# Kernel optimization log

Measured on AMD Instinct MI355X. Metric: run time of the kernel, lower is better.

## Reference

```python
import jax, jax.numpy as jnp
import numpy as np

N = 50000
E = 800000
H = 128


def _lin_init(key, fan_in, fan_out):
    s = 1.0 / np.sqrt(fan_in)
    k1, k2 = jax.random.split(key)
    W = jax.random.uniform(k1, (fan_in, fan_out), minval=-s, maxval=s, dtype=jnp.float32)
    b = jax.random.uniform(k2, (fan_out,), minval=-s, maxval=s, dtype=jnp.float32)
    return W, b


def setup_inputs() -> dict:
    key = jax.random.key(0)
    ks = jax.random.split(key, 24)
    inp = {}
    inp['x'] = jax.random.normal(ks[0], (N, 1), dtype=jnp.float32)
    inp['edge_attr'] = jax.random.normal(ks[1], (E, 1), dtype=jnp.float32)
    inp['q_Y_sample'] = jax.random.normal(ks[2], (E, 1), dtype=jnp.float32)
    inp['adj'] = jax.random.randint(ks[3], (2, E), 0, N, dtype=jnp.int32)
    inp['t'] = jax.random.uniform(ks[4], (1,), dtype=jnp.float32) * 1000.0
    inp['num_steps'] = 1000
    inp['batch'] = jnp.zeros((N,), dtype=jnp.int32)
    # parameters
    inp['We'], inp['be'] = _lin_init(ks[5], 1, H // 2)      # edge_map
    inp['Wo'], inp['bo'] = _lin_init(ks[6], 1, H // 2)      # edge_map_opt
    inp['Wl1'], inp['bl1'] = _lin_init(ks[7], H, 1)         # conv1 edge lin (edge_dim->in_channels)
    inp['Wn1'], inp['bn1'] = _lin_init(ks[8], 1, H)         # conv1 nn
    inp['Wl2'], inp['bl2'] = _lin_init(ks[9], H, H)         # conv2 edge lin
    inp['Wn2'], inp['bn2'] = _lin_init(ks[10], H, H)        # conv2 nn
    inp['Wl3'], inp['bl3'] = _lin_init(ks[11], H, H)        # conv3 edge lin
    inp['Wn3'], inp['bn3'] = _lin_init(ks[12], H, H)        # conv3 nn
    inp['Wt1'], inp['bt1'] = _lin_init(ks[13], H, 2 * H)    # time_mlp[0]
    inp['Wt2'], inp['bt2'] = _lin_init(ks[14], 2 * H, H)    # time_mlp[2]
    inp['Wd1'], inp['bd1'] = _lin_init(ks[15], 257, 257)    # decode[0]
    inp['Wd2'], inp['bd2'] = _lin_init(ks[16], 257, 1)      # decode[2]
    return inp


def reference(x, edge_attr, q_Y_sample, adj, t, num_steps, batch,
              We, be, Wo, bo,
              Wl1, bl1, Wn1, bn1, Wl2, bl2, Wn2, bn2, Wl3, bl3, Wn3, bn3,
              Wt1, bt1, Wt2, bt2, Wd1, bd1, Wd2, bd2):
    n = x.shape[0]
    src, dst = adj[0], adj[1]
    # edge embedding: cat(edge_map(edge_attr), edge_map_opt(q_Y_sample)) -> [E, 128]
    ee = jnp.concatenate([edge_attr @ We + be, q_Y_sample @ Wo + bo], axis=-1)
    # sinusoidal time embedding (t/num_steps*num_steps*rescale == 4*t)
    half = H // 2
    freqs = jnp.exp(jnp.arange(half, dtype=jnp.float32) * (-np.log(10000.0) / (half - 1)))
    tv = (t * 4.0)[:, None] * freqs[None, :]
    temb = jnp.concatenate([jnp.sin(tv), jnp.cos(tv)], axis=-1)  # [1, 128]
    temb = jax.nn.relu(temb @ Wt1 + bt1) @ Wt2 + bt2              # [1, 128], broadcasts to [N, 128]

    def gine(h, Wl, bl, Wn, bn):
        # PyG GINEConv (eps=0): out = nn(x + sum_j relu(x_j + lin(edge_attr)))
        m = jax.nn.relu(h[src] + (ee @ Wl + bl))                  # [E, d_in]
        agg = jax.ops.segment_sum(m, dst, num_segments=n)         # [N, d_in]
        return (h + agg) @ Wn + bn

    h = gine(x, Wl1, bl1, Wn1, bn1) + temb
    h = gine(h, Wl2, bl2, Wn2, bn2) + temb
    h = gine(h, Wl3, bl3, Wn3, bn3) + temb
    # decode on edges: cat(h[src], h[dst], q_Y_sample) -> MLP -> [E, 1]
    z = jnp.concatenate([h[src], h[dst], q_Y_sample], axis=-1)    # [E, 257]
    return jax.nn.relu(z @ Wd1 + bd1) @ Wd2 + bd2
```

## Files before the change

kernel.cpp:

```cpp
#include <hip/hip_runtime.h>

typedef unsigned int uint;
typedef unsigned short ushort;

#define AB_U 132

typedef __attribute__((ext_vector_type(8))) short short8;
typedef __attribute__((ext_vector_type(4))) float f32x4;
union U4S8 { uint4 u; short8 s; };

__device__ __forceinline__ ushort f2bf(float f) {
    uint u = __float_as_uint(f);
    u += 0x7FFFu + ((u >> 16) & 1u);
    return (ushort)(u >> 16);
}
__device__ __forceinline__ float bf2f_lo(uint p) { return __uint_as_float(p << 16); }
__device__ __forceinline__ float bf2f_hi(uint p) { return __uint_as_float(p & 0xFFFF0000u); }
__device__ __forceinline__ uint packbf(float lo, float hi) {
    return (uint)f2bf(lo) | ((uint)f2bf(hi) << 16);
}

__global__ __launch_bounds__(256) void precompute_kernel(
    const float* __restrict__ t,
    const float* __restrict__ We, const float* __restrict__ be,
    const float* __restrict__ Wo, const float* __restrict__ bo,
    const float* __restrict__ Wl1, const float* __restrict__ bl1,
    const float* __restrict__ Wl2, const float* __restrict__ bl2,
    const float* __restrict__ Wl3, const float* __restrict__ bl3,
    const float* __restrict__ Wt1, const float* __restrict__ bt1,
    const float* __restrict__ Wt2, const float* __restrict__ bt2,
    float* __restrict__ wsmall)
{
    __shared__ float t0[128];
    __shared__ float y1[256];
    int tid = threadIdx.x;
    float tt = t[0] * 4.0f;
    if (tid < 64) {
        float f = expf(-logf(10000.0f) * (float)tid / 63.0f);
        float v = tt * f;
        t0[tid]      = sinf(v);
        t0[tid + 64] = cosf(v);
    }
    __syncthreads();
    {
        float acc = bt1[tid];
        for (int k = 0; k < 128; k++) acc = fmaf(t0[k], Wt1[k * 256 + tid], acc);
        y1[tid] = fmaxf(acc, 0.0f);
    }
    __syncthreads();
    if (tid < 128) {
        float a = bt2[tid];
        for (int k = 0; k < 256; k++) a = fmaf(y1[k], Wt2[k * 128 + tid], a);
        wsmall[tid] = a;
    }
    {
        int j = tid & 127;
        const float* Wl  = (tid < 128) ? Wl2 : Wl3;
        const float* blp = (tid < 128) ? bl2 : bl3;
        float p = 0.f, q = 0.f, r = blp[j];
        for (int k = 0; k < 64; k++) {
            float w1 = Wl[k * 128 + j], w2 = Wl[(64 + k) * 128 + j];
            p = fmaf(We[k], w1, p);
            q = fmaf(Wo[k], w2, q);
            r = fmaf(be[k], w1, r);
            r = fmaf(bo[k], w2, r);
        }
        int base = (tid < 128) ? 128 : 512;
        wsmall[base + j]       = p;
        wsmall[base + 128 + j] = q;
        wsmall[base + 256 + j] = r;
    }
    if (tid == 0) {
        float p1 = 0.f, q1 = 0.f, r1 = bl1[0];
        for (int k = 0; k < 64; k++) {
            p1 = fmaf(We[k], Wl1[k], p1);
            q1 = fmaf(Wo[k], Wl1[64 + k], q1);
            r1 = fmaf(be[k], Wl1[k], r1);
            r1 = fmaf(bo[k], Wl1[64 + k], r1);
        }
        wsmall[896] = p1; wsmall[897] = q1; wsmall[898] = r1;
    }
}

__global__ __launch_bounds__(64) void wt16_kernel(
    const float* __restrict__ Wd1, uint* __restrict__ Wt16u)
{
    int c = blockIdx.x;
    int u = threadIdx.x;
    int k = u * 2;
    float lo, hi;
    if (c < 256) {
        lo = Wd1[k * 257 + c];
        hi = Wd1[(k + 1) * 257 + c];
    } else {
        int cc = c - 256;
        lo = Wd1[(128 + k) * 257 + cc];
        hi = Wd1[(128 + k + 1) * 257 + cc];
    }
    Wt16u[c * 64 + u] = packbf(lo, hi);
}

__global__ __launch_bounds__(64) void wnt16_kernel(
    const float* __restrict__ W, uint* __restrict__ Wt)
{
    int c = blockIdx.x, u = threadIdx.x;
    Wt[c * 64 + u] = packbf(W[(2 * u) * 128 + c], W[(2 * u + 1) * 128 + c]);
}

__global__ __launch_bounds__(256) void hist_kernel(
    const int* __restrict__ dst, int* __restrict__ cnt, int E)
{
    int e = blockIdx.x * blockDim.x + threadIdx.x;
    if (e < E) atomicAdd(&cnt[dst[e]], 1);
}

__global__ __launch_bounds__(256) void scan1_kernel(
    const int* __restrict__ cnt, int* __restrict__ rowstart,
    int* __restrict__ partials, int N)
{
    __shared__ int wsum[4];
    int b = blockIdx.x;
    int tid = threadIdx.x, lane = tid & 63, w = tid >> 6;
    int i0 = b * 1024 + tid * 4;
    int v0 = (i0     < N) ? cnt[i0]     : 0;
    int v1 = (i0 + 1 < N) ? cnt[i0 + 1] : 0;
    int v2 = (i0 + 2 < N) ? cnt[i0 + 2] : 0;
    int v3 = (i0 + 3 < N) ? cnt[i0 + 3] : 0;
    int tsum = v0 + v1 + v2 + v3;
    int s = tsum;
#pragma unroll
    for (int off = 1; off < 64; off <<= 1) {
        int u = __shfl_up(s, off, 64);
        if (lane >= off) s += u;
    }
    if (lane == 63) wsum[w] = s;
    __syncthreads();
    int woff = 0;
    for (int k = 0; k < w; k++) woff += wsum[k];
    int ex = woff + s - tsum;
    if (i0     < N) rowstart[i0]     = ex;
    if (i0 + 1 < N) rowstart[i0 + 1] = ex + v0;
    if (i0 + 2 < N) rowstart[i0 + 2] = ex + v0 + v1;
    if (i0 + 3 < N) rowstart[i0 + 3] = ex + v0 + v1 + v2;
    if (tid == 255) partials[b] = woff + s;
}

__global__ __launch_bounds__(64) void scan2_kernel(
    int* __restrict__ partials, int* __restrict__ rowstart, int nblk, int N)
{
    int lane = threadIdx.x;
    int carry = 0;
    for (int base = 0; base < nblk; base += 64) {
        int i = base + lane;
        int v = (i < nblk) ? partials[i] : 0;
        int s = v;
#pragma unroll
        for (int off = 1; off < 64; off <<= 1) {
            int u = __shfl_up(s, off, 64);
            if (lane >= off) s += u;
        }
        if (i < nblk) partials[i] = carry + s - v;
        carry += __shfl(s, 63, 64);
    }
    if (lane == 0) rowstart[N] = carry;
}

__global__ __launch_bounds__(256) void scan3_kernel(
    int* __restrict__ rowstart, const int* __restrict__ partials, int N)
{
    int i = blockIdx.x * blockDim.x + threadIdx.x;
    if (i < N) rowstart[i] += partials[i >> 10];
}

__global__ __launch_bounds__(256) void scatter_kernel(
    const int* __restrict__ src, const int* __restrict__ dst,
    const float* __restrict__ ea, const float* __restrict__ qy,
    const int* __restrict__ rowstart, int* __restrict__ cursor,
    uint4* __restrict__ epack, int E)
{
    int e = blockIdx.x * blockDim.x + threadIdx.x;
    if (e >= E) return;
    int d = dst[e];
    int pos = atomicAdd(&cursor[d], 1);
    uint4 pk;
    pk.x = (uint)e;
    pk.y = (uint)src[e];
    pk.z = __float_as_uint(ea[e]);
    pk.w = __float_as_uint(qy[e]);
    epack[rowstart[d] + pos] = pk;
}

__global__ __launch_bounds__(256) void edge1_kernel(
    const float* __restrict__ x, const uint4* __restrict__ epack,
    const int* __restrict__ rowstart, const float* __restrict__ scal,
    float* __restrict__ agg1, int N)
{
    int v = blockIdx.x * blockDim.x + threadIdx.x;
    if (v >= N) return;
    float s0 = scal[0], s1 = scal[1], s2 = scal[2];
    int beg = rowstart[v], end = rowstart[v + 1];
    float m = 0.0f;
    int i = beg;
    for (; i + 2 <= end; i += 2) {
        uint4 pk0 = epack[i];
        uint4 pk1 = epack[i + 1];
        float x0 = x[(int)pk0.y];
        float x1 = x[(int)pk1.y];
        m += fmaxf(x0 + fmaf(__uint_as_float(pk0.z), s0, fmaf(__uint_as_float(pk0.w), s1, s2)), 0.0f);
        m += fmaxf(x1 + fmaf(__uint_as_float(pk1.z), s0, fmaf(__uint_as_float(pk1.w), s1, s2)), 0.0f);
    }
    if (i < end) {
        uint4 pk = epack[i];
        m += fmaxf(x[(int)pk.y] + fmaf(__uint_as_float(pk.z), s0, fmaf(__uint_as_float(pk.w), s1, s2)), 0.0f);
    }
    agg1[v] = m;
}

__global__ __launch_bounds__(256) void node1_kernel(
    const float* __restrict__ x, const float* __restrict__ agg1,
    const float* __restrict__ Wn1, const float* __restrict__ bn1,
    const float* __restrict__ temb, uint* __restrict__ h16u, int N)
{
    int i = blockIdx.x * blockDim.x + threadIdx.x;
    int n = i >> 6, j2 = (i & 63) * 2;
    if (n >= N) return;
    float v = x[n] + agg1[n];
    float h0 = fmaf(v, Wn1[j2],     bn1[j2]     + temb[j2]);
    float h1 = fmaf(v, Wn1[j2 + 1], bn1[j2 + 1] + temb[j2 + 1]);
    h16u[(size_t)n * 64 + (j2 >> 1)] = packbf(h0, h1);
}

__global__ __launch_bounds__(256) void aggL_kernel(
    const uint* __restrict__ h16u, const uint4* __restrict__ epack,
    const int* __restrict__ rowstart,
    const float* __restrict__ P, const float* __restrict__ Q,
    const float* __restrict__ R, uint* __restrict__ agg16u, int N)
{
    int v = blockIdx.x * 4 + (threadIdx.x >> 6);
    int lane = threadIdx.x & 63;
    if (v >= N) return;
    int c = lane * 2;
    float2 Pv = *(const float2*)(P + c);
    float2 Qv = *(const float2*)(Q + c);
    float2 Rv = *(const float2*)(R + c);
    int beg = rowstart[v], end = rowstart[v + 1];
    float accx = 0.0f, accy = 0.0f;
    int i = beg;
    for (; i + 8 <= end; i += 8) {
        uint4 pk[8];
        uint hp[8];
#pragma unroll
        for (int j = 0; j < 8; j++) pk[j] = epack[i + j];
#pragma unroll
        for (int j = 0; j < 8; j++) hp[j] = h16u[(size_t)pk[j].y * 64 + lane];
#pragma unroll
        for (int j = 0; j < 8; j++) {
            float a = __uint_as_float(pk[j].z), b = __uint_as_float(pk[j].w);
            accx += fmaxf(bf2f_lo(hp[j]) + fmaf(a, Pv.x, fmaf(b, Qv.x, Rv.x)), 0.0f);
            accy += fmaxf(bf2f_hi(hp[j]) + fmaf(a, Pv.y, fmaf(b, Qv.y, Rv.y)), 0.0f);
        }
    }
    for (; i + 2 <= end; i += 2) {
        uint4 pk0 = epack[i];
        uint4 pk1 = epack[i + 1];
        uint hp0 = h16u[(size_t)pk0.y * 64 + lane];
        uint hp1 = h16u[(size_t)pk1.y * 64 + lane];
        float a0 = __uint_as_float(pk0.z), b0 = __uint_as_float(pk0.w);
        float a1 = __uint_as_float(pk1.z), b1 = __uint_as_float(pk1.w);
        accx += fmaxf(bf2f_lo(hp0) + fmaf(a0, Pv.x, fmaf(b0, Qv.x, Rv.x)), 0.0f);
        accy += fmaxf(bf2f_hi(hp0) + fmaf(a0, Pv.y, fmaf(b0, Qv.y, Rv.y)), 0.0f);
        accx += fmaxf(bf2f_lo(hp1) + fmaf(a1, Pv.x, fmaf(b1, Qv.x, Rv.x)), 0.0f);
        accy += fmaxf(bf2f_hi(hp1) + fmaf(a1, Pv.y, fmaf(b1, Qv.y, Rv.y)), 0.0f);
    }
    if (i < end) {
        uint4 pk = epack[i];
        float a = __uint_as_float(pk.z), b = __uint_as_float(pk.w);
        uint hp = h16u[(size_t)pk.y * 64 + lane];
        accx += fmaxf(bf2f_lo(hp) + fmaf(a, Pv.x, fmaf(b, Qv.x, Rv.x)), 0.0f);
        accy += fmaxf(bf2f_hi(hp) + fmaf(a, Pv.y, fmaf(b, Qv.y, Rv.y)), 0.0f);
    }
    agg16u[(size_t)v * 64 + lane] = packbf(accx, accy);
}

__global__ __launch_bounds__(256) void nodeL_kernel(
    const uint* __restrict__ agg16u, const uint* __restrict__ Wn2t16u,
    const float* __restrict__ bn, const float* __restrict__ temb,
    uint* __restrict__ h16u, int N)
{
    __shared__ uint vs16[64][68];
    int nb = blockIdx.x * 64;
    int tid = threadIdx.x;
    for (int idx = tid; idx < 64 * 32; idx += 256) {
        int n = idx >> 5, u2 = (idx & 31) * 2;
        uint2 pk = make_uint2(0, 0);
        if (nb + n < N) {
            uint2 hp = *(const uint2*)(h16u + (size_t)(nb + n) * 64 + u2);
            uint2 gp = *(const uint2*)(agg16u + (size_t)(nb + n) * 64 + u2);
            pk.x = packbf(bf2f_lo(hp.x) + bf2f_lo(gp.x), bf2f_hi(hp.x) + bf2f_hi(gp.x));
            pk.y = packbf(bf2f_lo(hp.y) + bf2f_lo(gp.y), bf2f_hi(hp.y) + bf2f_hi(gp.y));
        }
        *(uint2*)(&vs16[n][u2]) = pk;
    }
    __syncthreads();
    int wv = tid >> 6, lane = tid & 63, cl = lane & 15, g = lane >> 4;
    int rbase = wv * 16;
    short8 afr[4];
#pragma unroll
    for (int kc = 0; kc < 4; kc++) {
        U4S8 t;
        t.u = *(const uint4*)(&vs16[rbase + cl][kc * 16 + g * 4]);
        afr[kc] = t.s;
    }
#pragma unroll
    for (int tt = 0; tt < 8; tt++) {
        int c = tt * 16 + cl;
        float bias = bn[c] + temb[c];
        f32x4 acc = {bias, bias, bias, bias};
#pragma unroll
        for (int kc = 0; kc < 4; kc++) {
            U4S8 t;
            t.u = *(const uint4*)(Wn2t16u + (size_t)c * 64 + kc * 16 + g * 4);
            acc = __builtin_amdgcn_mfma_f32_16x16x32_bf16(afr[kc], t.s, acc, 0, 0, 0);
        }
#pragma unroll
        for (int r = 0; r < 4; r++) {
            int n = nb + rbase + g * 4 + r;
            float val = acc[r];
            float nbr = __shfl_down(val, 1, 64);
            if (n < N && (cl & 1) == 0)
                h16u[(size_t)n * 64 + (c >> 1)] = packbf(val, nbr);
        }
    }
}

__global__ __launch_bounds__(256) void node3_decode_kernel(
    const uint* __restrict__ h16u, const uint* __restrict__ agg16u,
    const uint* __restrict__ Wn3t16u, const float* __restrict__ bn3,
    const float* __restrict__ temb, const uint* __restrict__ Wt16u,
    const float* __restrict__ Wd1, const float* __restrict__ bd1,
    uint* __restrict__ A16u, uint* __restrict__ B16u, int N)
{
    __shared__ uint vs16[16][68];
    __shared__ float hs3[16][132];
    __shared__ uint stA[16 * 132];
    __shared__ uint stB[16 * 132];
    int nb = blockIdx.x * 16;
    int tid = threadIdx.x;
    for (int idx = tid; idx < 16 * 32; idx += 256) {
        int n = idx >> 5, u2 = (idx & 31) * 2;
        uint2 pk = make_uint2(0, 0);
        if (nb + n < N) {
            uint2 hp = *(const uint2*)(h16u + (size_t)(nb + n) * 64 + u2);
            uint2 gp = *(const uint2*)(agg16u + (size_t)(nb + n) * 64 + u2);
            pk.x = packbf(bf2f_lo(hp.x) + bf2f_lo(gp.x), bf2f_hi(hp.x) + bf2f_hi(gp.x));
            pk.y = packbf(bf2f_lo(hp.y) + bf2f_lo(gp.y), bf2f_hi(hp.y) + bf2f_hi(gp.y));
        }
        *(uint2*)(&vs16[n][u2]) = pk;
    }
    __syncthreads();
    int wv = tid >> 6, lane = tid & 63, cl = lane & 15, g = lane >> 4;
    {
        short8 afr[4];
#pragma unroll
        for (int kc = 0; kc < 4; kc++) {
            U4S8 t;
            t.u = *(const uint4*)(&vs16[cl][kc * 16 + g * 4]);
            afr[kc] = t.s;
        }
#pragma unroll
        for (int tt = 0; tt < 2; tt++) {
            int c = wv * 32 + tt * 16 + cl;
            float bias = bn3[c] + temb[c];
            f32x4 acc = {bias, bias, bias, bias};
#pragma unroll
            for (int kc = 0; kc < 4; kc++) {
                U4S8 t;
                t.u = *(const uint4*)(Wn3t16u + (size_t)c * 64 + kc * 16 + g * 4);
                acc = __builtin_amdgcn_mfma_f32_16x16x32_bf16(afr[kc], t.s, acc, 0, 0, 0);
            }
#pragma unroll
            for (int r = 0; r < 4; r++) hs3[g * 4 + r][c] = acc[r];
        }
    }
    __syncthreads();
    {
        short8 afr[4];
#pragma unroll
        for (int kc = 0; kc < 4; kc++) {
            float4 lo = *(const float4*)(&hs3[cl][kc * 32 + g * 8]);
            float4 hi = *(const float4*)(&hs3[cl][kc * 32 + g * 8 + 4]);
            U4S8 t;
            t.u.x = packbf(lo.x, lo.y);
            t.u.y = packbf(lo.z, lo.w);
            t.u.z = packbf(hi.x, hi.y);
            t.u.w = packbf(hi.z, hi.w);
            afr[kc] = t.s;
        }
#pragma unroll
        for (int tt = 0; tt < 8; tt++) {
            int tile = wv * 8 + tt;
            int c = tile * 16 + cl;
            float bias = (tile < 16) ? bd1[c] : 0.0f;
            f32x4 acc = {bias, bias, bias, bias};
#pragma unroll
            for (int kc = 0; kc < 4; kc++) {
                U4S8 t;
                t.u = *(const uint4*)(Wt16u + (size_t)c * 64 + kc * 16 + g * 4);
                acc = __builtin_amdgcn_mfma_f32_16x16x32_bf16(afr[kc], t.s, acc, 0, 0, 0);
            }
            ushort* SP = (ushort*)((tile < 16) ? stA : stB);
            int oc = (tile < 16) ? c : (c - 256);
#pragma unroll
            for (int r = 0; r < 4; r++)
                SP[(g * 4 + r) * 264 + oc] = f2bf(acc[r]);
        }
    }
    if (tid < 64) {
        int n = tid >> 2, j = tid & 3;
        float sA = 0.f, sB = 0.f;
        for (int k = j * 32; k < j * 32 + 32; k++) {
            float hv = hs3[n][k];
            sA = fmaf(hv, Wd1[k * 257 + 256], sA);
            sB = fmaf(hv, Wd1[(128 + k) * 257 + 256], sB);
        }
        sA += __shfl_xor(sA, 1, 64);
        sA += __shfl_xor(sA, 2, 64);
        sB += __shfl_xor(sB, 1, 64);
        sB += __shfl_xor(sB, 2, 64);
        if (j == 0) {
            ((ushort*)stA)[n * 264 + 256] = f2bf(sA + bd1[256]);
            ((ushort*)stB)[n * 264 + 256] = f2bf(sB);
        }
    }
    __syncthreads();
    {
        int rows = N - nb; if (rows > 16) rows = 16;
        int tot2 = rows * 66;
        uint2* gA = (uint2*)(A16u + (size_t)nb * AB_U);
        uint2* gB = (uint2*)(B16u + (size_t)nb * AB_U);
        const uint2* sA = (const uint2*)stA;
        const uint2* sB = (const uint2*)stB;
        for (int idx = tid; idx < tot2; idx += 256) {
            gA[idx] = sA[idx];
            gB[idx] = sB[idx];
        }
    }
}

__global__ __launch_bounds__(256) void decodeE_kernel(
    const uint* __restrict__ A16u, const uint* __restrict__ B16u,
    const uint4* __restrict__ epack, const int* __restrict__ rowstart,
    const float* __restrict__ Wd1, const float* __restrict__ Wd2,
    const float* __restrict__ bd2, float* __restrict__ out, int N)
{
    int v = blockIdx.x * 4 + (threadIdx.x >> 6);
    int lane = threadIdx.x & 63;
    if (v >= N) return;
    const float* w256 = Wd1 + 256 * 257;
    float4 w2v = *(const float4*)(w256 + lane * 4);
    float4 wdv = *(const float4*)(Wd2 + lane * 4);
    const uint* Br = B16u + (size_t)v * AB_U;
    uint2 bp = *(const uint2*)(Br + lane * 2);
    float Bv0 = bf2f_lo(bp.x), Bv1 = bf2f_hi(bp.x);
    float Bv2 = bf2f_lo(bp.y), Bv3 = bf2f_hi(bp.y);
    float w2_l = w256[256], wd_l = Wd2[256], bd = bd2[0];
    float B_l = bf2f_lo(Br[128]);
    int beg = rowstart[v], end = rowstart[v + 1];
    int i = beg;
    for (; i + 4 <= end; i += 4) {
        uint4 pk[4];
        uint2 ap[4];
#pragma unroll
        for (int j = 0; j < 4; j++) pk[j] = epack[i + j];
#pragma unroll
        for (int j = 0; j < 4; j++)
            ap[j] = *(const uint2*)(A16u + (size_t)pk[j].y * AB_U + lane * 2);
        float acc[4];
#pragma unroll
        for (int j = 0; j < 4; j++) {
            float q = __uint_as_float(pk[j].w);
            float y0 = bf2f_lo(ap[j].x) + fmaf(q, w2v.x, Bv0);
            float y1 = bf2f_hi(ap[j].x) + fmaf(q, w2v.y, Bv1);
            float y2 = bf2f_lo(ap[j].y) + fmaf(q, w2v.z, Bv2);
            float y3 = bf2f_hi(ap[j].y) + fmaf(q, w2v.w, Bv3);
            acc[j] = fmaxf(y0, 0.f) * wdv.x + fmaxf(y1, 0.f) * wdv.y
                   + fmaxf(y2, 0.f) * wdv.z + fmaxf(y3, 0.f) * wdv.w;
        }
        int l1 = lane & 1, l2 = lane & 2;
        float s01 = l1 ? acc[0] : acc[1];
        float r01 = __shfl_xor(s01, 1, 64);
        float a01 = (l1 ? acc[1] : acc[0]) + r01;
        float s23 = l1 ? acc[2] : acc[3];
        float r23 = __shfl_xor(s23, 1, 64);
        float a23 = (l1 ? acc[3] : acc[2]) + r23;
        float sb = l2 ? a01 : a23;
        float rb = __shfl_xor(sb, 2, 64);
        float b = (l2 ? a23 : a01) + rb;
        b += __shfl_xor(b, 4, 64);
        b += __shfl_xor(b, 8, 64);
        b += __shfl_xor(b, 16, 64);
        b += __shfl_xor(b, 32, 64);
        uint ssel = l2 ? (l1 ? pk[3].y : pk[2].y) : (l1 ? pk[1].y : pk[0].y);
        uint esel = l2 ? (l1 ? pk[3].x : pk[2].x) : (l1 ? pk[1].x : pk[0].x);
        uint qsel = l2 ? (l1 ? pk[3].w : pk[2].w) : (l1 ? pk[1].w : pk[0].w);
        if (lane < 4) {
            float tl = bf2f_lo(A16u[(size_t)ssel * AB_U + 128]);
            float q = __uint_as_float(qsel);
            float tail = fmaxf(tl + fmaf(q, w2_l, B_l), 0.f) * wd_l;
            out[(int)esel] = b + tail + bd;
        }
    }
    for (; i < end; i++) {
        uint4 pk = epack[i];
        float q = __uint_as_float(pk.w);
        const uint* Ar = A16u + (size_t)pk.y * AB_U;
        uint2 ap = *(const uint2*)(Ar + lane * 2);
        float y0 = bf2f_lo(ap.x) + fmaf(q, w2v.x, Bv0);
        float y1 = bf2f_hi(ap.x) + fmaf(q, w2v.y, Bv1);
        float y2 = bf2f_lo(ap.y) + fmaf(q, w2v.z, Bv2);
        float y3 = bf2f_hi(ap.y) + fmaf(q, w2v.w, Bv3);
        float acc = fmaxf(y0, 0.f) * wdv.x + fmaxf(y1, 0.f) * wdv.y
                  + fmaxf(y2, 0.f) * wdv.z + fmaxf(y3, 0.f) * wdv.w;
        if (lane == 0) {
            float yl = bf2f_lo(Ar[128]) + fmaf(q, w2_l, B_l);
            acc = fmaf(fmaxf(yl, 0.f), wd_l, acc);
        }
#pragma unroll
        for (int off = 32; off > 0; off >>= 1) acc += __shfl_xor(acc, off, 64);
        if (lane == 0) out[(int)pk.x] = acc + bd;
    }
}

extern "C" void kernel_launch(void* const* d_in, const int* in_sizes, int n_in,
                              void* d_out, int out_size, void* d_ws, size_t ws_size,
                              hipStream_t stream) {
    (void)n_in; (void)out_size; (void)ws_size;
    const float* x   = (const float*)d_in[0];
    const float* ea  = (const float*)d_in[1];
    const float* qy  = (const float*)d_in[2];
    const int*   adj = (const int*)d_in[3];
    const float* t   = (const float*)d_in[4];
    const float* We  = (const float*)d_in[7];
    const float* be  = (const float*)d_in[8];
    const float* Wo  = (const float*)d_in[9];
    const float* bo  = (const float*)d_in[10];
    const float* Wl1 = (const float*)d_in[11];
    const float* bl1 = (const float*)d_in[12];
    const float* Wn1 = (const float*)d_in[13];
    const float* bn1 = (const float*)d_in[14];
    const float* Wl2 = (const float*)d_in[15];
    const float* bl2 = (const float*)d_in[16];
    const float* Wn2 = (const float*)d_in[17];
    const float* bn2 = (const float*)d_in[18];
    const float* Wl3 = (const float*)d_in[19];
    const float* bl3 = (const float*)d_in[20];
    const float* Wn3 = (const float*)d_in[21];
    const float* bn3 = (const float*)d_in[22];
    const float* Wt1 = (const float*)d_in[23];
    const float* bt1 = (const float*)d_in[24];
    const float* Wt2 = (const float*)d_in[25];
    const float* bt2 = (const float*)d_in[26];
    const float* Wd1 = (const float*)d_in[27];
    const float* bd1 = (const float*)d_in[28];
    const float* Wd2 = (const float*)d_in[29];
    const float* bd2 = (const float*)d_in[30];
    float* out = (float*)d_out;

    int N = in_sizes[0];
    int E = in_sizes[3] / 2;
    const int* src = adj;
    const int* dst = adj + E;

    float* w    = (float*)d_ws;
    float* temb = w;
    float* P2   = w + 128;
    float* Q2   = w + 256;
    float* R2   = w + 384;
    float* P3   = w + 512;
    float* Q3   = w + 640;
    float* R3   = w + 768;
    float* scal = w + 896;
    float* agg1 = w + 1024;
    uint*  h16u   = (uint*)(agg1 + N);
    uint*  agg16u = h16u + (size_t)N * 64;
    uint*  A16u   = agg16u + (size_t)N * 64;
    uint*  B16u   = A16u + (size_t)N * AB_U;
    int* rowstart = (int*)(B16u + (size_t)N * AB_U);
    int* cursor   = rowstart + (N + 1);
    int* partials = cursor + N;
    int nblk = (N + 1023) / 1024;
    char* pcur = (char*)(partials + nblk + 1);
    pcur = (char*)(((uintptr_t)pcur + 15) & ~(uintptr_t)15);
    uint4* epack = (uint4*)pcur;
    uint* Wt16u   = (uint*)(epack + E);
    uint* Wn2t16u = Wt16u + 512 * 64;
    uint* Wn3t16u = Wn2t16u + 128 * 64;

    hipMemsetAsync(cursor, 0, (size_t)N * sizeof(int), stream);
    hist_kernel<<<(E + 255) / 256, 256, 0, stream>>>(dst, cursor, E);
    scan1_kernel<<<nblk, 256, 0, stream>>>(cursor, rowstart, partials, N);
    scan2_kernel<<<1, 64, 0, stream>>>(partials, rowstart, nblk, N);
    scan3_kernel<<<(N + 255) / 256, 256, 0, stream>>>(rowstart, partials, N);
    hipMemsetAsync(cursor, 0, (size_t)N * sizeof(int), stream);
    scatter_kernel<<<(E + 255) / 256, 256, 0, stream>>>(src, dst, ea, qy, rowstart, cursor, epack, E);

    wt16_kernel<<<512, 64, 0, stream>>>(Wd1, Wt16u);
    wnt16_kernel<<<128, 64, 0, stream>>>(Wn2, Wn2t16u);
    wnt16_kernel<<<128, 64, 0, stream>>>(Wn3, Wn3t16u);
    precompute_kernel<<<1, 256, 0, stream>>>(t, We, be, Wo, bo, Wl1, bl1,
                                             Wl2, bl2, Wl3, bl3,
                                             Wt1, bt1, Wt2, bt2, w);
    edge1_kernel<<<(N + 255) / 256, 256, 0, stream>>>(x, epack, rowstart, scal, agg1, N);
    node1_kernel<<<(N * 64 + 255) / 256, 256, 0, stream>>>(x, agg1, Wn1, bn1, temb, h16u, N);
    aggL_kernel<<<(N + 3) / 4, 256, 0, stream>>>(h16u, epack, rowstart, P2, Q2, R2, agg16u, N);
    nodeL_kernel<<<(N + 63) / 64, 256, 0, stream>>>(agg16u, Wn2t16u, bn2, temb, h16u, N);
    aggL_kernel<<<(N + 3) / 4, 256, 0, stream>>>(h16u, epack, rowstart, P3, Q3, R3, agg16u, N);
    node3_decode_kernel<<<(N + 15) / 16, 256, 0, stream>>>(h16u, agg16u, Wn3t16u, bn3, temb,
                                                           Wt16u, Wd1, bd1,
                                                           A16u, B16u, N);
    decodeE_kernel<<<(N + 3) / 4, 256, 0, stream>>>(A16u, B16u, epack, rowstart, Wd1, Wd2, bd2, out, N);
}
```

Baseline: 522.0 us.

## Fuse edge aggregation into node GEMM kernels and merge weight staging kernels

Edge aggregation for layers 2 and 3 now runs inside the node-update kernels, which use 1024-thread blocks: one wave aggregates one node, then the block runs the MFMA GEMM on the 16 aggregated rows held in shared memory. This removes the agg16u round trip through global memory and two kernel launches. Ping-pong hA/hB buffers avoid read-after-write hazards. The three weight-transpose kernels are merged into one launch. In exchange, large blocks with only 8 or 4 of 16 waves active in the GEMM phase may lower occupancy and leave waves idle while the slowest node's gather finishes.

```diff
diff --git a/kernel.cpp b/kernel.cpp
--- a/kernel.cpp
+++ b/kernel.cpp
@@ -82,29 +82,24 @@
     }
 }
 
-__global__ __launch_bounds__(64) void wt16_kernel(
-    const float* __restrict__ Wd1, uint* __restrict__ Wt16u)
-{
-    int c = blockIdx.x;
-    int u = threadIdx.x;
-    int k = u * 2;
-    float lo, hi;
+__global__ __launch_bounds__(64) void stage_kernel(
+    const float* __restrict__ Wd1, const float* __restrict__ Wn2,
+    const float* __restrict__ Wn3, uint* __restrict__ Wt16u,
+    uint* __restrict__ Wn2t16u, uint* __restrict__ Wn3t16u)
+{
+    int c = blockIdx.x, u = threadIdx.x, k = u * 2;
     if (c < 256) {
-        lo = Wd1[k * 257 + c];
-        hi = Wd1[(k + 1) * 257 + c];
+        Wt16u[c * 64 + u] = packbf(Wd1[k * 257 + c], Wd1[(k + 1) * 257 + c]);
+    } else if (c < 512) {
+        int cc = c - 256;
+        Wt16u[c * 64 + u] = packbf(Wd1[(128 + k) * 257 + cc], Wd1[(128 + k + 1) * 257 + cc]);
+    } else if (c < 640) {
+        int cc = c - 512;
+        Wn2t16u[cc * 64 + u] = packbf(Wn2[k * 128 + cc], Wn2[(k + 1) * 128 + cc]);
     } else {
-        int cc = c - 256;
-        lo = Wd1[(128 + k) * 257 + cc];
-        hi = Wd1[(128 + k + 1) * 257 + cc];
-    }
-    Wt16u[c * 64 + u] = packbf(lo, hi);
-}
-
-__global__ __launch_bounds__(64) void wnt16_kernel(
-    const float* __restrict__ W, uint* __restrict__ Wt)
-{
-    int c = blockIdx.x, u = threadIdx.x;
-    Wt[c * 64 + u] = packbf(W[(2 * u) * 128 + c], W[(2 * u + 1) * 128 + c]);
+        int cc = c - 640;
+        Wn3t16u[cc * 64 + u] = packbf(Wn3[k * 128 + cc], Wn3[(k + 1) * 128 + cc]);
+    }
 }
 
 __global__ __launch_bounds__(256) void hist_kernel(
@@ -230,21 +225,11 @@
     h16u[(size_t)n * 64 + (j2 >> 1)] = packbf(h0, h1);
 }
 
-__global__ __launch_bounds__(256) void aggL_kernel(
-    const uint* __restrict__ h16u, const uint4* __restrict__ epack,
-    const int* __restrict__ rowstart,
-    const float* __restrict__ P, const float* __restrict__ Q,
-    const float* __restrict__ R, uint* __restrict__ agg16u, int N)
-{
-    int v = blockIdx.x * 4 + (threadIdx.x >> 6);
-    int lane = threadIdx.x & 63;
-    if (v >= N) return;
-    int c = lane * 2;
-    float2 Pv = *(const float2*)(P + c);
-    float2 Qv = *(const float2*)(Q + c);
-    float2 Rv = *(const float2*)(R + c);
-    int beg = rowstart[v], end = rowstart[v + 1];
-    float accx = 0.0f, accy = 0.0f;
+__device__ __forceinline__ void agg_node(
+    const uint* __restrict__ hsrc, const uint4* __restrict__ epack,
+    int beg, int end, int lane, float2 Pv, float2 Qv, float2 Rv,
+    float& accx, float& accy)
+{
     int i = beg;
     for (; i + 8 <= end; i += 8) {
         uint4 pk[8];
@@ -252,7 +237,7 @@
 #pragma unroll
         for (int j = 0; j < 8; j++) pk[j] = epack[i + j];
 #pragma unroll
-        for (int j = 0; j < 8; j++) hp[j] = h16u[(size_t)pk[j].y * 64 + lane];
+        for (int j = 0; j < 8; j++) hp[j] = hsrc[(size_t)pk[j].y * 64 + lane];
 #pragma unroll
         for (int j = 0; j < 8; j++) {
             float a = __uint_as_float(pk[j].z), b = __uint_as_float(pk[j].w);
@@ -263,8 +248,8 @@
     for (; i + 2 <= end; i += 2) {
         uint4 pk0 = epack[i];
         uint4 pk1 = epack[i + 1];
-        uint hp0 = h16u[(size_t)pk0.y * 64 + lane];
-        uint hp1 = h16u[(size_t)pk1.y * 64 + lane];
+        uint hp0 = hsrc[(size_t)pk0.y * 64 + lane];
+        uint hp1 = hsrc[(size_t)pk1.y * 64 + lane];
         float a0 = __uint_as_float(pk0.z), b0 = __uint_as_float(pk0.w);
         float a1 = __uint_as_float(pk1.z), b1 = __uint_as_float(pk1.w);
         accx += fmaxf(bf2f_lo(hp0) + fmaf(a0, Pv.x, fmaf(b0, Qv.x, Rv.x)), 0.0f);
@@ -275,45 +260,49 @@
     if (i < end) {
         uint4 pk = epack[i];
         float a = __uint_as_float(pk.z), b = __uint_as_float(pk.w);
-        uint hp = h16u[(size_t)pk.y * 64 + lane];
+        uint hp = hsrc[(size_t)pk.y * 64 + lane];
         accx += fmaxf(bf2f_lo(hp) + fmaf(a, Pv.x, fmaf(b, Qv.x, Rv.x)), 0.0f);
         accy += fmaxf(bf2f_hi(hp) + fmaf(a, Pv.y, fmaf(b, Qv.y, Rv.y)), 0.0f);
     }
-    agg16u[(size_t)v * 64 + lane] = packbf(accx, accy);
-}
-
-__global__ __launch_bounds__(256) void nodeL_kernel(
-    const uint* __restrict__ agg16u, const uint* __restrict__ Wn2t16u,
+}
+
+__global__ __launch_bounds__(1024) void aggnode2_kernel(
+    const uint* __restrict__ hA, const uint4* __restrict__ epack,
+    const int* __restrict__ rowstart,
+    const float* __restrict__ P, const float* __restrict__ Q,
+    const float* __restrict__ R, const uint* __restrict__ Wn2t16u,
     const float* __restrict__ bn, const float* __restrict__ temb,
-    uint* __restrict__ h16u, int N)
-{
-    __shared__ uint vs16[64][68];
-    int nb = blockIdx.x * 64;
+    uint* __restrict__ hB, int N)
+{
+    __shared__ uint vs16[16][68];
+    int nb = blockIdx.x * 16;
     int tid = threadIdx.x;
-    for (int idx = tid; idx < 64 * 32; idx += 256) {
-        int n = idx >> 5, u2 = (idx & 31) * 2;
-        uint2 pk = make_uint2(0, 0);
-        if (nb + n < N) {
-            uint2 hp = *(const uint2*)(h16u + (size_t)(nb + n) * 64 + u2);
-            uint2 gp = *(const uint2*)(agg16u + (size_t)(nb + n) * 64 + u2);
-            pk.x = packbf(bf2f_lo(hp.x) + bf2f_lo(gp.x), bf2f_hi(hp.x) + bf2f_hi(gp.x));
-            pk.y = packbf(bf2f_lo(hp.y) + bf2f_lo(gp.y), bf2f_hi(hp.y) + bf2f_hi(gp.y));
-        }
-        *(uint2*)(&vs16[n][u2]) = pk;
+    int w = tid >> 6, lane = tid & 63;
+    int v = nb + w;
+    {
+        int c = lane * 2;
+        float2 Pv = *(const float2*)(P + c);
+        float2 Qv = *(const float2*)(Q + c);
+        float2 Rv = *(const float2*)(R + c);
+        float accx = 0.0f, accy = 0.0f;
+        uint hp = 0;
+        if (v < N) {
+            agg_node(hA, epack, rowstart[v], rowstart[v + 1], lane, Pv, Qv, Rv, accx, accy);
+            hp = hA[(size_t)v * 64 + lane];
+        }
+        vs16[w][lane] = packbf(bf2f_lo(hp) + accx, bf2f_hi(hp) + accy);
     }
     __syncthreads();
-    int wv = tid >> 6, lane = tid & 63, cl = lane & 15, g = lane >> 4;
-    int rbase = wv * 16;
-    short8 afr[4];
-#pragma unroll
-    for (int kc = 0; kc < 4; kc++) {
-        U4S8 t;
-        t.u = *(const uint4*)(&vs16[rbase + cl][kc * 16 + g * 4]);
-        afr[kc] = t.s;
-    }
-#pragma unroll
-    for (int tt = 0; tt < 8; tt++) {
-        int c = tt * 16 + cl;
+    if (w < 8) {
+        int cl = lane & 15, g = lane >> 4;
+        short8 afr[4];
+#pragma unroll
+        for (int kc = 0; kc < 4; kc++) {
+            U4S8 t;
+            t.u = *(const uint4*)(&vs16[cl][kc * 16 + g * 4]);
+            afr[kc] = t.s;
+        }
+        int c = w * 16 + cl;
         float bias = bn[c] + temb[c];
         f32x4 acc = {bias, bias, bias, bias};
 #pragma unroll
@@ -324,21 +313,24 @@
         }
 #pragma unroll
         for (int r = 0; r < 4; r++) {
-            int n = nb + rbase + g * 4 + r;
+            int n = nb + g * 4 + r;
             float val = acc[r];
             float nbr = __shfl_down(val, 1, 64);
             if (n < N && (cl & 1) == 0)
-                h16u[(size_t)n * 64 + (c >> 1)] = packbf(val, nbr);
-        }
-    }
-}
-
-__global__ __launch_bounds__(256) void node3_decode_kernel(
-    const uint* __restrict__ h16u, const uint* __restrict__ agg16u,
-    const uint* __restrict__ Wn3t16u, const float* __restrict__ bn3,
-    const float* __restrict__ temb, const uint* __restrict__ Wt16u,
-    const float* __restrict__ Wd1, const float* __restrict__ bd1,
-    uint* __restrict__ A16u, uint* __restrict__ B16u, int N)
+                hB[(size_t)n * 64 + (c >> 1)] = packbf(val, nbr);
+        }
+    }
+}
+
+__global__ __launch_bounds__(1024) void aggnode3_kernel(
+    const uint* __restrict__ hB, const uint4* __restrict__ epack,
+    const int* __restrict__ rowstart,
+    const float* __restrict__ P, const float* __restrict__ Q,
+    const float* __restrict__ R, const uint* __restrict__ Wn3t16u,
+    const float* __restrict__ bn3, const float* __restrict__ temb,
+    const uint* __restrict__ Wt16u, const float* __restrict__ Wd1,
+    const float* __restrict__ bd1, uint* __restrict__ A16u,
+    uint* __restrict__ B16u, int N)
 {
     __shared__ uint vs16[16][68];
     __shared__ float hs3[16][132];
@@ -346,20 +338,24 @@
     __shared__ uint stB[16 * 132];
     int nb = blockIdx.x * 16;
     int tid = threadIdx.x;
-    for (int idx = tid; idx < 16 * 32; idx += 256) {
-        int n = idx >> 5, u2 = (idx & 31) * 2;
-        uint2 pk = make_uint2(0, 0);
-        if (nb + n < N) {
-            uint2 hp = *(const uint2*)(h16u + (size_t)(nb + n) * 64 + u2);
-            uint2 gp = *(const uint2*)(agg16u + (size_t)(nb + n) * 64 + u2);
-            pk.x = packbf(bf2f_lo(hp.x) + bf2f_lo(gp.x), bf2f_hi(hp.x) + bf2f_hi(gp.x));
-            pk.y = packbf(bf2f_lo(hp.y) + bf2f_lo(gp.y), bf2f_hi(hp.y) + bf2f_hi(gp.y));
-        }
-        *(uint2*)(&vs16[n][u2]) = pk;
+    int w = tid >> 6, lane = tid & 63;
+    int v = nb + w;
+    {
+        int c = lane * 2;
+        float2 Pv = *(const float2*)(P + c);
+        float2 Qv = *(const float2*)(Q + c);
+        float2 Rv = *(const float2*)(R + c);
+        float accx = 0.0f, accy = 0.0f;
+        uint hp = 0;
+        if (v < N) {
+            agg_node(hB, epack, rowstart[v], rowstart[v + 1], lane, Pv, Qv, Rv, accx, accy);
+            hp = hB[(size_t)v * 64 + lane];
+        }
+        vs16[w][lane] = packbf(bf2f_lo(hp) + accx, bf2f_hi(hp) + accy);
     }
     __syncthreads();
-    int wv = tid >> 6, lane = tid & 63, cl = lane & 15, g = lane >> 4;
-    {
+    if (tid < 256) {
+        int wv = w, cl = lane & 15, g = lane >> 4;
         short8 afr[4];
 #pragma unroll
         for (int kc = 0; kc < 4; kc++) {
@@ -383,7 +379,8 @@
         }
     }
     __syncthreads();
-    {
+    if (tid < 256) {
+        int wv = w, cl = lane & 15, g = lane >> 4;
         short8 afr[4];
 #pragma unroll
         for (int kc = 0; kc < 4; kc++) {
@@ -440,7 +437,7 @@
         uint2* gB = (uint2*)(B16u + (size_t)nb * AB_U);
         const uint2* sA = (const uint2*)stA;
         const uint2* sB = (const uint2*)stB;
-        for (int idx = tid; idx < tot2; idx += 256) {
+        for (int idx = tid; idx < tot2; idx += 1024) {
             gA[idx] = sA[idx];
             gB[idx] = sB[idx];
         }
@@ -581,9 +578,9 @@
     float* R3   = w + 768;
     float* scal = w + 896;
     float* agg1 = w + 1024;
-    uint*  h16u   = (uint*)(agg1 + N);
-    uint*  agg16u = h16u + (size_t)N * 64;
-    uint*  A16u   = agg16u + (size_t)N * 64;
+    uint*  hA     = (uint*)(agg1 + N);
+    uint*  hB     = hA + (size_t)N * 64;
+    uint*  A16u   = hB + (size_t)N * 64;
     uint*  B16u   = A16u + (size_t)N * AB_U;
     int* rowstart = (int*)(B16u + (size_t)N * AB_U);
     int* cursor   = rowstart + (N + 1);
@@ -604,19 +601,16 @@
     hipMemsetAsync(cursor, 0, (size_t)N * sizeof(int), stream);
     scatter_kernel<<<(E + 255) / 256, 256, 0, stream>>>(src, dst, ea, qy, rowstart, cursor, epack, E);
 
-    wt16_kernel<<<512, 64, 0, stream>>>(Wd1, Wt16u);
-    wnt16_kernel<<<128, 64, 0, stream>>>(Wn2, Wn2t16u);
-    wnt16_kernel<<<128, 64, 0, stream>>>(Wn3, Wn3t16u);
+    stage_kernel<<<768, 64, 0, stream>>>(Wd1, Wn2, Wn3, Wt16u, Wn2t16u, Wn3t16u);
     precompute_kernel<<<1, 256, 0, stream>>>(t, We, be, Wo, bo, Wl1, bl1,
                                              Wl2, bl2, Wl3, bl3,
                                              Wt1, bt1, Wt2, bt2, w);
     edge1_kernel<<<(N + 255) / 256, 256, 0, stream>>>(x, epack, rowstart, scal, agg1, N);
-    node1_kernel<<<(N * 64 + 255) / 256, 256, 0, stream>>>(x, agg1, Wn1, bn1, temb, h16u, N);
-    aggL_kernel<<<(N + 3) / 4, 256, 0, stream>>>(h16u, epack, rowstart, P2, Q2, R2, agg16u, N);
-    nodeL_kernel<<<(N + 63) / 64, 256, 0, stream>>>(agg16u, Wn2t16u, bn2, temb, h16u, N);
-    aggL_kernel<<<(N + 3) / 4, 256, 0, stream>>>(h16u, epack, rowstart, P3, Q3, R3, agg16u, N);
-    node3_decode_kernel<<<(N + 15) / 16, 256, 0, stream>>>(h16u, agg16u, Wn3t16u, bn3, temb,
-                                                           Wt16u, Wd1, bd1,
-                                                           A16u, B16u, N);
+    node1_kernel<<<(N * 64 + 255) / 256, 256, 0, stream>>>(x, agg1, Wn1, bn1, temb, hA, N);
+    aggnode2_kernel<<<(N + 15) / 16, 1024, 0, stream>>>(hA, epack, rowstart, P2, Q2, R2,
+                                                        Wn2t16u, bn2, temb, hB, N);
+    aggnode3_kernel<<<(N + 15) / 16, 1024, 0, stream>>>(hB, epack, rowstart, P3, Q3, R3,
+                                                        Wn3t16u, bn3, temb, Wt16u, Wd1, bd1,
+                                                        A16u, B16u, N);
     decodeE_kernel<<<(N + 3) / 4, 256, 0, stream>>>(A16u, B16u, epack, rowstart, Wd1, Wd2, bd2, out, N);
 }
```

Result: slower. 559.6 us (+7.2%).

## Exploit rank-1 layer-1 output to gather scalars instead of 128-wide features

Applied to the files above, without the earlier changes.

Layer 1's output h1 = v*Wn1 + bn1 + temb is rank-1 in the per-node scalar v = x + agg1. The node1 kernel is dropped, and layer 2's aggregation now gathers one float per edge and rebuilds h1 on the fly. This replaces a 256-byte bf16 row gather per edge with a 4-byte gather and removes writing and reading the h16 buffer. In exchange each edge does one extra FMA per channel, and the gather loop is unrolled by 8 for more loads in flight. The three weight-conversion kernels are also merged into one launch.

```diff
diff --git a/kernel.cpp b/kernel.cpp
--- a/kernel.cpp
+++ b/kernel.cpp
@@ -82,29 +82,24 @@
     }
 }
 
-__global__ __launch_bounds__(64) void wt16_kernel(
-    const float* __restrict__ Wd1, uint* __restrict__ Wt16u)
-{
-    int c = blockIdx.x;
-    int u = threadIdx.x;
-    int k = u * 2;
-    float lo, hi;
+__global__ __launch_bounds__(64) void stage_kernel(
+    const float* __restrict__ Wd1, const float* __restrict__ Wn2,
+    const float* __restrict__ Wn3, uint* __restrict__ Wt16u,
+    uint* __restrict__ Wn2t16u, uint* __restrict__ Wn3t16u)
+{
+    int c = blockIdx.x, u = threadIdx.x, k = u * 2;
     if (c < 256) {
-        lo = Wd1[k * 257 + c];
-        hi = Wd1[(k + 1) * 257 + c];
+        Wt16u[c * 64 + u] = packbf(Wd1[k * 257 + c], Wd1[(k + 1) * 257 + c]);
+    } else if (c < 512) {
+        int cc = c - 256;
+        Wt16u[c * 64 + u] = packbf(Wd1[(128 + k) * 257 + cc], Wd1[(128 + k + 1) * 257 + cc]);
+    } else if (c < 640) {
+        int cc = c - 512;
+        Wn2t16u[cc * 64 + u] = packbf(Wn2[k * 128 + cc], Wn2[(k + 1) * 128 + cc]);
     } else {
-        int cc = c - 256;
-        lo = Wd1[(128 + k) * 257 + cc];
-        hi = Wd1[(128 + k + 1) * 257 + cc];
-    }
-    Wt16u[c * 64 + u] = packbf(lo, hi);
-}
-
-__global__ __launch_bounds__(64) void wnt16_kernel(
-    const float* __restrict__ W, uint* __restrict__ Wt)
-{
-    int c = blockIdx.x, u = threadIdx.x;
-    Wt[c * 64 + u] = packbf(W[(2 * u) * 128 + c], W[(2 * u + 1) * 128 + c]);
+        int cc = c - 640;
+        Wn3t16u[cc * 64 + u] = packbf(Wn3[k * 128 + cc], Wn3[(k + 1) * 128 + cc]);
+    }
 }
 
 __global__ __launch_bounds__(256) void hist_kernel(
@@ -193,7 +188,7 @@
 __global__ __launch_bounds__(256) void edge1_kernel(
     const float* __restrict__ x, const uint4* __restrict__ epack,
     const int* __restrict__ rowstart, const float* __restrict__ scal,
-    float* __restrict__ agg1, int N)
+    float* __restrict__ vout, int N)
 {
     int v = blockIdx.x * blockDim.x + threadIdx.x;
     if (v >= N) return;
@@ -213,21 +208,52 @@
         uint4 pk = epack[i];
         m += fmaxf(x[(int)pk.y] + fmaf(__uint_as_float(pk.z), s0, fmaf(__uint_as_float(pk.w), s1, s2)), 0.0f);
     }
-    agg1[v] = m;
-}
-
-__global__ __launch_bounds__(256) void node1_kernel(
-    const float* __restrict__ x, const float* __restrict__ agg1,
-    const float* __restrict__ Wn1, const float* __restrict__ bn1,
-    const float* __restrict__ temb, uint* __restrict__ h16u, int N)
-{
-    int i = blockIdx.x * blockDim.x + threadIdx.x;
-    int n = i >> 6, j2 = (i & 63) * 2;
-    if (n >= N) return;
-    float v = x[n] + agg1[n];
-    float h0 = fmaf(v, Wn1[j2],     bn1[j2]     + temb[j2]);
-    float h1 = fmaf(v, Wn1[j2 + 1], bn1[j2 + 1] + temb[j2 + 1]);
-    h16u[(size_t)n * 64 + (j2 >> 1)] = packbf(h0, h1);
+    vout[v] = x[v] + m;
+}
+
+__global__ __launch_bounds__(256) void aggL2v_kernel(
+    const float* __restrict__ v, const uint4* __restrict__ epack,
+    const int* __restrict__ rowstart,
+    const float* __restrict__ P, const float* __restrict__ Q,
+    const float* __restrict__ R, const float* __restrict__ Wn1,
+    const float* __restrict__ bn1, const float* __restrict__ temb,
+    uint* __restrict__ agg16u, int N)
+{
+    int vn = blockIdx.x * 4 + (threadIdx.x >> 6);
+    int lane = threadIdx.x & 63;
+    if (vn >= N) return;
+    int c = lane * 2;
+    float2 Pv = *(const float2*)(P + c);
+    float2 Qv = *(const float2*)(Q + c);
+    float2 Rv = *(const float2*)(R + c);
+    float2 w1 = *(const float2*)(Wn1 + c);
+    Rv.x += bn1[c] + temb[c];
+    Rv.y += bn1[c + 1] + temb[c + 1];
+    int beg = rowstart[vn], end = rowstart[vn + 1];
+    float accx = 0.0f, accy = 0.0f;
+    int i = beg;
+    for (; i + 8 <= end; i += 8) {
+        uint4 pk[8];
+        float vv[8];
+#pragma unroll
+        for (int j = 0; j < 8; j++) pk[j] = epack[i + j];
+#pragma unroll
+        for (int j = 0; j < 8; j++) vv[j] = v[(int)pk[j].y];
+#pragma unroll
+        for (int j = 0; j < 8; j++) {
+            float a = __uint_as_float(pk[j].z), b = __uint_as_float(pk[j].w);
+            accx += fmaxf(fmaf(vv[j], w1.x, fmaf(a, Pv.x, fmaf(b, Qv.x, Rv.x))), 0.0f);
+            accy += fmaxf(fmaf(vv[j], w1.y, fmaf(a, Pv.y, fmaf(b, Qv.y, Rv.y))), 0.0f);
+        }
+    }
+    for (; i < end; i++) {
+        uint4 pk = epack[i];
+        float a = __uint_as_float(pk.z), b = __uint_as_float(pk.w);
+        float vv = v[(int)pk.y];
+        accx += fmaxf(fmaf(vv, w1.x, fmaf(a, Pv.x, fmaf(b, Qv.x, Rv.x))), 0.0f);
+        accy += fmaxf(fmaf(vv, w1.y, fmaf(a, Pv.y, fmaf(b, Qv.y, Rv.y))), 0.0f);
+    }
+    agg16u[(size_t)vn * 64 + lane] = packbf(accx, accy);
 }
 
 __global__ __launch_bounds__(256) void aggL_kernel(
@@ -283,23 +309,26 @@
 }
 
 __global__ __launch_bounds__(256) void nodeL_kernel(
-    const uint* __restrict__ agg16u, const uint* __restrict__ Wn2t16u,
-    const float* __restrict__ bn, const float* __restrict__ temb,
-    uint* __restrict__ h16u, int N)
+    const float* __restrict__ v, const float* __restrict__ Wn1,
+    const float* __restrict__ bn1, const uint* __restrict__ agg16u,
+    const uint* __restrict__ Wn2t16u, const float* __restrict__ bn,
+    const float* __restrict__ temb, uint* __restrict__ hB, int N)
 {
     __shared__ uint vs16[64][68];
     int nb = blockIdx.x * 64;
     int tid = threadIdx.x;
-    for (int idx = tid; idx < 64 * 32; idx += 256) {
-        int n = idx >> 5, u2 = (idx & 31) * 2;
-        uint2 pk = make_uint2(0, 0);
+    for (int idx = tid; idx < 64 * 64; idx += 256) {
+        int n = idx >> 6, l = idx & 63;
+        uint pk = 0;
         if (nb + n < N) {
-            uint2 hp = *(const uint2*)(h16u + (size_t)(nb + n) * 64 + u2);
-            uint2 gp = *(const uint2*)(agg16u + (size_t)(nb + n) * 64 + u2);
-            pk.x = packbf(bf2f_lo(hp.x) + bf2f_lo(gp.x), bf2f_hi(hp.x) + bf2f_hi(gp.x));
-            pk.y = packbf(bf2f_lo(hp.y) + bf2f_lo(gp.y), bf2f_hi(hp.y) + bf2f_hi(gp.y));
-        }
-        *(uint2*)(&vs16[n][u2]) = pk;
+            float vv = v[nb + n];
+            uint gp = agg16u[(size_t)(nb + n) * 64 + l];
+            int c = l * 2;
+            float h0 = fmaf(vv, Wn1[c],     bn1[c]     + temb[c])     + bf2f_lo(gp);
+            float h1 = fmaf(vv, Wn1[c + 1], bn1[c + 1] + temb[c + 1]) + bf2f_hi(gp);
+            pk = packbf(h0, h1);
+        }
+        vs16[n][l] = pk;
     }
     __syncthreads();
     int wv = tid >> 6, lane = tid & 63, cl = lane & 15, g = lane >> 4;
@@ -328,7 +357,7 @@
             float val = acc[r];
             float nbr = __shfl_down(val, 1, 64);
             if (n < N && (cl & 1) == 0)
-                h16u[(size_t)n * 64 + (c >> 1)] = packbf(val, nbr);
+                hB[(size_t)n * 64 + (c >> 1)] = packbf(val, nbr);
         }
     }
 }
@@ -580,9 +609,9 @@
     float* Q3   = w + 640;
     float* R3   = w + 768;
     float* scal = w + 896;
-    float* agg1 = w + 1024;
-    uint*  h16u   = (uint*)(agg1 + N);
-    uint*  agg16u = h16u + (size_t)N * 64;
+    float* v    = w + 1024;
+    uint*  hB     = (uint*)(v + N);
+    uint*  agg16u = hB + (size_t)N * 64;
     uint*  A16u   = agg16u + (size_t)N * 64;
     uint*  B16u   = A16u + (size_t)N * AB_U;
     int* rowstart = (int*)(B16u + (size_t)N * AB_U);
@@ -604,18 +633,17 @@
     hipMemsetAsync(cursor, 0, (size_t)N * sizeof(int), stream);
     scatter_kernel<<<(E + 255) / 256, 256, 0, stream>>>(src, dst, ea, qy, rowstart, cursor, epack, E);
 
-    wt16_kernel<<<512, 64, 0, stream>>>(Wd1, Wt16u);
-    wnt16_kernel<<<128, 64, 0, stream>>>(Wn2, Wn2t16u);
-    wnt16_kernel<<<128, 64, 0, stream>>>(Wn3, Wn3t16u);
+    stage_kernel<<<768, 64, 0, stream>>>(Wd1, Wn2, Wn3, Wt16u, Wn2t16u, Wn3t16u);
     precompute_kernel<<<1, 256, 0, stream>>>(t, We, be, Wo, bo, Wl1, bl1,
                                              Wl2, bl2, Wl3, bl3,
                                              Wt1, bt1, Wt2, bt2, w);
-    edge1_kernel<<<(N + 255) / 256, 256, 0, stream>>>(x, epack, rowstart, scal, agg1, N);
-    node1_kernel<<<(N * 64 + 255) / 256, 256, 0, stream>>>(x, agg1, Wn1, bn1, temb, h16u, N);
-    aggL_kernel<<<(N + 3) / 4, 256, 0, stream>>>(h16u, epack, rowstart, P2, Q2, R2, agg16u, N);
-    nodeL_kernel<<<(N + 63) / 64, 256, 0, stream>>>(agg16u, Wn2t16u, bn2, temb, h16u, N);
-    aggL_kernel<<<(N + 3) / 4, 256, 0, stream>>>(h16u, epack, rowstart, P3, Q3, R3, agg16u, N);
-    node3_decode_kernel<<<(N + 15) / 16, 256, 0, stream>>>(h16u, agg16u, Wn3t16u, bn3, temb,
+    edge1_kernel<<<(N + 255) / 256, 256, 0, stream>>>(x, epack, rowstart, scal, v, N);
+    aggL2v_kernel<<<(N + 3) / 4, 256, 0, stream>>>(v, epack, rowstart, P2, Q2, R2,
+                                                   Wn1, bn1, temb, agg16u, N);
+    nodeL_kernel<<<(N + 63) / 64, 256, 0, stream>>>(v, Wn1, bn1, agg16u, Wn2t16u,
+                                                    bn2, temb, hB, N);
+    aggL_kernel<<<(N + 3) / 4, 256, 0, stream>>>(hB, epack, rowstart, P3, Q3, R3, agg16u, N);
+    node3_decode_kernel<<<(N + 15) / 16, 256, 0, stream>>>(hB, agg16u, Wn3t16u, bn3, temb,
                                                            Wt16u, Wd1, bd1,
                                                            A16u, B16u, N);
     decodeE_kernel<<<(N + 3) / 4, 256, 0, stream>>>(A16u, B16u, epack, rowstart, Wd1, Wd2, bd2, out, N);
```

Result: faster. 503.2 us (-3.6%).
